# Kernel optimization log

Hardware: AMD Instinct MI355X
Metric: run time of the kernel (lower is better)

Reference implementation:

```python
import jax, jax.numpy as jnp
import numpy as np

N = 100000   # nodes
E = 1600000  # edges
G = 512      # graphs
H = 128      # hidden = dim_features
T = 10       # dim_target
L = 4        # no_layers (first_h + 3 GINConvs)
BN_EPS = 1e-5


def setup_inputs() -> dict:
    key = jax.random.key(0)
    ks = jax.random.split(key, 12)
    s = 1.0 / np.sqrt(H)
    inp = {
        "x": jax.random.normal(ks[0], (N, H), jnp.float32),
        "edge_index": jax.random.randint(ks[1], (2, E), 0, N, jnp.int64),
        "batch": jnp.sort(jax.random.randint(ks[2], (N,), 0, G, jnp.int64)),
        "Wa": jax.random.normal(ks[3], (L, H, H), jnp.float32) * s,
        "ba": jax.random.normal(ks[4], (L, H), jnp.float32) * s,
        "ga": jnp.ones((L, H), jnp.float32),
        "bea": jnp.zeros((L, H), jnp.float32),
        "Wb": jax.random.normal(ks[5], (L, H, H), jnp.float32) * s,
        "bb": jax.random.normal(ks[6], (L, H), jnp.float32) * s,
        "gb": jnp.ones((L, H), jnp.float32),
        "beb": jnp.zeros((L, H), jnp.float32),
        "Wl": jax.random.normal(ks[7], (L, H, T), jnp.float32) * s,
        "bl": jax.random.normal(ks[8], (L, T), jnp.float32) * s,
        "eps": jnp.zeros((3,), jnp.float32),
    }
    return inp


def _bn(h, g, b):
    # BatchNorm1d in training mode: batch stats over node dim, biased var
    mu = jnp.mean(h, axis=0)
    var = jnp.mean(jnp.square(h - mu), axis=0)
    return g * (h - mu) * jax.lax.rsqrt(var + BN_EPS) + b


def _mlp(h, l, Wa, ba, ga, bea, Wb, bb, gb, beb):
    # Linear -> BN -> ReLU -> Linear -> BN -> ReLU
    h = jax.nn.relu(_bn(h @ Wa[l] + ba[l], ga[l], bea[l]))
    h = jax.nn.relu(_bn(h @ Wb[l] + bb[l], gb[l], beb[l]))
    return h


def _mean_pool(v, batch):
    sums = jax.ops.segment_sum(v, batch, num_segments=G)
    cnt = jax.ops.segment_sum(jnp.ones((v.shape[0], 1), v.dtype), batch, num_segments=G)
    return sums / jnp.maximum(cnt, 1.0)


def reference(x, edge_index, batch, Wa, ba, ga, bea, Wb, bb, gb, beb, Wl, bl, eps):
    src, dst = edge_index[0], edge_index[1]
    # layer 0: first_h MLP, then linear -> pool
    h = _mlp(x, 0, Wa, ba, ga, bea, Wb, bb, gb, beb)
    out = _mean_pool(h @ Wl[0] + bl[0], batch)
    # layers 1..3: GINConv = MLP((1+eps)*x + sum_{j->i} x_j), then pool -> linear
    for l in range(1, L):
        agg = jax.ops.segment_sum(h[src], dst, num_segments=N)  # scatter-add over edges
        h = _mlp((1.0 + eps[l - 1]) * h + agg, l, Wa, ba, ga, bea, Wb, bb, gb, beb)
        out = out + _mean_pool(h, batch) @ Wl[l] + bl[l]
    return jax.nn.sigmoid(out.reshape(-1))  # [G*T]
```

## Files before the change

### kernel.cpp

```cpp
#include <hip/hip_runtime.h>
#include <hip/hip_bf16.h>

#define N_      100000
#define E_      1600000
#define G_      512
#define H_      128
#define T_      10
#define BN_EPS  1e-5f
#define SP_     16

#define NB_     782
#define NBLK_   256
#define ECHUNK_ 6250
#define SCANN_  (NB_ * NBLK_)
#define SCANB_  ((SCANN_ + 1023) / 1024)

typedef __attribute__((ext_vector_type(8))) short short8;
typedef __attribute__((ext_vector_type(4))) float floatx4;

__device__ __forceinline__ float bf2f(short s) {
    return __uint_as_float(((unsigned int)(unsigned short)s) << 16);
}
__device__ __forceinline__ short f2bf(float f) {
    unsigned int u = __float_as_uint(f);
    u += 0x7fffu + ((u >> 16) & 1u);
    return (short)(u >> 16);
}

__global__ __launch_bounds__(256) void prep(
    const float* __restrict__ Wa, const float* __restrict__ Wb,
    short* __restrict__ Wt, const int* __restrict__ edst,
    int* __restrict__ BH)
{
    __shared__ int hist[NB_];
    const int t = threadIdx.x, blk = blockIdx.x;
    for (int i = t; i < NB_; i += 256) hist[i] = 0;
    __syncthreads();

    for (int i = blk * 256 + t; i < 8 * 16384; i += NBLK_ * 256) {
        int mat = i >> 14;
        int rem = i & 16383;
        int n = rem >> 7;
        int k = rem & 127;
        const float* W = (mat < 4) ? (Wa + (size_t)mat * 16384)
                                   : (Wb + (size_t)(mat - 4) * 16384);
        Wt[(size_t)mat * 16384 + n * 128 + k] = f2bf(W[k * 128 + n]);
    }
    const int base = blk * ECHUNK_;
    for (int i = base + t; i < base + ECHUNK_; i += 256)
        atomicAdd(&hist[edst[i] >> 7], 1);
    __syncthreads();
    for (int b = t; b < NB_; b += 256)
        BH[b * NBLK_ + blk] = hist[b];
}

__global__ __launch_bounds__(256) void scan1(const int* __restrict__ X,
                                             int* __restrict__ Y,
                                             int* __restrict__ bsum, int n)
{
    __shared__ int sd[256];
    int t = threadIdx.x;
    int base = blockIdx.x * 1024 + t * 4;
    int c0 = (base + 0 < n) ? X[base + 0] : 0;
    int c1 = (base + 1 < n) ? X[base + 1] : 0;
    int c2 = (base + 2 < n) ? X[base + 2] : 0;
    int c3 = (base + 3 < n) ? X[base + 3] : 0;
    int s = c0 + c1 + c2 + c3;
    sd[t] = s;
    __syncthreads();
    for (int d = 1; d < 256; d <<= 1) {
        int v = (t >= d) ? sd[t - d] : 0;
        __syncthreads();
        sd[t] += v;
        __syncthreads();
    }
    int p = sd[t] - s;
    if (base + 0 < n) Y[base + 0] = p;
    if (base + 1 < n) Y[base + 1] = p + c0;
    if (base + 2 < n) Y[base + 2] = p + c0 + c1;
    if (base + 3 < n) Y[base + 3] = p + c0 + c1 + c2;
    if (t == 255) bsum[blockIdx.x] = sd[255];
}

__device__ __forceinline__ void scan_bsum(const int* __restrict__ bsum,
                                          int* bexcl)
{
    int t = threadIdx.x;
    int v = (t < SCANB_) ? bsum[t] : 0;
    bexcl[t] = v;
    __syncthreads();
    for (int d = 1; d < 256; d <<= 1) {
        int u = (t >= d) ? bexcl[t - d] : 0;
        __syncthreads();
        bexcl[t] += u;
        __syncthreads();
    }
    int inc = bexcl[t];
    __syncthreads();
    bexcl[t] = inc - v;
    __syncthreads();
}

__global__ __launch_bounds__(256) void scatter_ebuf(
    const int* __restrict__ esrc, const int* __restrict__ edst,
    const int* __restrict__ BHs, const int* __restrict__ bsum,
    int* __restrict__ ebuf)
{
    __shared__ int sbuf[NB_];
    __shared__ int bexcl[256];
    const int t = threadIdx.x, blk = blockIdx.x;
    scan_bsum(bsum, bexcl);
    for (int b = t; b < NB_; b += 256)
        sbuf[b] = BHs[b * NBLK_ + blk] + bexcl[b >> 2];
    __syncthreads();
    const int base = blk * ECHUNK_;
    for (int i = base + t; i < base + ECHUNK_; i += 256) {
        int s = esrc[i], d = edst[i];
        int pos = atomicAdd(&sbuf[d >> 7], 1);
        ebuf[pos] = s | ((d & 127) << 17);
    }
}

__global__ __launch_bounds__(256) void fill_buckets(
    const int* __restrict__ ebuf, const int* __restrict__ BHs,
    const int* __restrict__ bsum, int* __restrict__ eidx,
    int* __restrict__ off)
{
    __shared__ int cnt[128];
    __shared__ int sc[256];
    __shared__ int bexcl[256];
    const int b = blockIdx.x, t = threadIdx.x;
    scan_bsum(bsum, bexcl);
    const int bstart = BHs[b * NBLK_] + bexcl[b >> 2];
    int bend = E_;
    if (b != NB_ - 1)
        bend = BHs[(b + 1) * NBLK_] + bexcl[(b + 1) >> 2];

    if (t < 128) cnt[t] = 0;
    __syncthreads();
    for (int i = bstart + t; i < bend; i += 256)
        atomicAdd(&cnt[(ebuf[i] >> 17) & 127], 1);
    __syncthreads();
    int v = (t < 128) ? cnt[t] : 0;
    sc[t] = v;
    __syncthreads();
    for (int d = 1; d < 128; d <<= 1) {
        int u = (t >= d) ? sc[t - d] : 0;
        __syncthreads();
        sc[t] += u;
        __syncthreads();
    }
    if (t < 128) {
        int node = (b << 7) + t;
        int pfx = sc[t] - v;
        if (node <= N_) off[node] = bstart + pfx;
        cnt[t] = bstart + pfx;
    }
    __syncthreads();
    for (int i = bstart + t; i < bend; i += 256) {
        int e = ebuf[i];
        int pos = atomicAdd(&cnt[(e >> 17) & 127], 1);
        eidx[pos] = e & 0x1FFFF;
    }
}

__global__ __launch_bounds__(512, 6) void gemm_mfma(
    const void* __restrict__ Ain, const short* __restrict__ Wt,
    const float* __restrict__ bias, short* __restrict__ Cout,
    float* __restrict__ statsOut,
    const float* __restrict__ statsIn, const float* __restrict__ gamma,
    const float* __restrict__ beta, int mode, int nrows)
{
    __shared__ __align__(16) short Bs[128][136];
    __shared__ float scale_s[128];
    __shared__ float shift_s[128];

    const int tid = threadIdx.x;

    {
        int r = tid >> 2;
        int part = (tid & 3) << 5;
        const short* g = Wt + r * 128 + part;
        short* d = &Bs[r][part];
#pragma unroll
        for (int i = 0; i < 4; ++i)
            *(short8*)(d + i * 8) = *(const short8*)(g + i * 8);
    }
    if (mode == 1 && tid < 128) {
        float s1 = 0.f, s2 = 0.f;
#pragma unroll
        for (int p = 0; p < SP_; ++p) {
            s1 += statsIn[p * 256 + tid];
            s2 += statsIn[p * 256 + 128 + tid];
        }
        const float nInv = 1.0f / (float)N_;
        float mu = s1 * nInv;
        float var = s2 * nInv - mu * mu;
        float sc = gamma[tid] * rsqrtf(var + BN_EPS);
        scale_s[tid] = sc;
        shift_s[tid] = beta[tid] - mu * sc;
    }
    __syncthreads();

    const int wave = tid >> 6;
    const int lane = tid & 63;
    const int m = lane & 15;
    const int quad = lane >> 4;
    const int rowBase = blockIdx.x * 128;
    const int row = rowBase + wave * 16 + m;
    const int arow = row < nrows ? row : nrows - 1;

    floatx4 acc[8];
#pragma unroll
    for (int i = 0; i < 8; ++i) acc[i] = (floatx4)0.f;

#pragma unroll
    for (int k0 = 0; k0 < 128; k0 += 32) {
        const int kb = k0 + quad * 8;
        short8 af;
        if (mode == 2) {
            const float* Af = (const float*)Ain + (size_t)arow * 128 + kb;
            float4 x0 = *(const float4*)(Af);
            float4 x1 = *(const float4*)(Af + 4);
            af[0] = f2bf(x0.x); af[1] = f2bf(x0.y);
            af[2] = f2bf(x0.z); af[3] = f2bf(x0.w);
            af[4] = f2bf(x1.x); af[5] = f2bf(x1.y);
            af[6] = f2bf(x1.z); af[7] = f2bf(x1.w);
        } else {
            af = *(const short8*)((const short*)Ain + (size_t)arow * 128 + kb);
            if (mode == 1) {
                float4 sc0 = *(const float4*)&scale_s[kb];
                float4 sc1 = *(const float4*)&scale_s[kb + 4];
                float4 sh0 = *(const float4*)&shift_s[kb];
                float4 sh1 = *(const float4*)&shift_s[kb + 4];
                af[0] = f2bf(fmaxf(fmaf(bf2f(af[0]), sc0.x, sh0.x), 0.f));
                af[1] = f2bf(fmaxf(fmaf(bf2f(af[1]), sc0.y, sh0.y), 0.f));
                af[2] = f2bf(fmaxf(fmaf(bf2f(af[2]), sc0.z, sh0.z), 0.f));
                af[3] = f2bf(fmaxf(fmaf(bf2f(af[3]), sc0.w, sh0.w), 0.f));
                af[4] = f2bf(fmaxf(fmaf(bf2f(af[4]), sc1.x, sh1.x), 0.f));
                af[5] = f2bf(fmaxf(fmaf(bf2f(af[5]), sc1.y, sh1.y), 0.f));
                af[6] = f2bf(fmaxf(fmaf(bf2f(af[6]), sc1.z, sh1.z), 0.f));
                af[7] = f2bf(fmaxf(fmaf(bf2f(af[7]), sc1.w, sh1.w), 0.f));
            }
        }
#pragma unroll
        for (int nt = 0; nt < 8; ++nt) {
            short8 bf = *(const short8*)&Bs[nt * 16 + m][kb];
            acc[nt] = __builtin_amdgcn_mfma_f32_16x16x32_bf16(af, bf, acc[nt], 0, 0, 0);
        }
    }

    float bv[8];
#pragma unroll
    for (int nt = 0; nt < 8; ++nt) bv[nt] = bias[nt * 16 + m];

    float (*Cs)[132] = (float(*)[132])&Bs[0][0];
    float S1 = 0.f, S2 = 0.f;
#pragma unroll
    for (int half = 0; half < 2; ++half) {
        __syncthreads();
        if ((wave >> 2) == half) {
            int wl = wave & 3;
#pragma unroll
            for (int nt = 0; nt < 8; ++nt)
#pragma unroll
                for (int r = 0; r < 4; ++r)
                    Cs[wl * 16 + quad * 4 + r][nt * 16 + m] = acc[nt][r] + bv[nt];
        }
        __syncthreads();
        {
            int trow = tid >> 3;
            int tcg = (tid & 7) << 4;
            int grow = rowBase + half * 64 + trow;
            if (grow < nrows) {
                short* dst = Cout + (size_t)grow * 128 + tcg;
                short8 o0, o1;
#pragma unroll
                for (int j = 0; j < 8; ++j) {
                    o0[j] = f2bf(Cs[trow][tcg + j]);
                    o1[j] = f2bf(Cs[trow][tcg + 8 + j]);
                }
                *(short8*)dst = o0;
                *(short8*)(dst + 8) = o1;
            }
        }
        if (tid < 128) {
            int nvalid = nrows - rowBase - half * 64;
            if (nvalid > 64) nvalid = 64;
            for (int r = 0; r < nvalid; ++r) {
                float v = Cs[r][tid];
                S1 += v; S2 += v * v;
            }
        }
    }
    if (tid < 128) {
        float* part = statsOut + ((blockIdx.x & (SP_ - 1)) << 8);
        atomicAdd(&part[tid], S1);
        atomicAdd(&part[128 + tid], S2);
    }
}

__global__ __launch_bounds__(128) void bn_relu_pool(
    const short* __restrict__ Cin, short* __restrict__ hout,
    const float* __restrict__ stats, const float* __restrict__ gamma,
    const float* __restrict__ beta, const int* __restrict__ batch,
    float* __restrict__ pooled, int n)
{
    int c = threadIdx.x;
    float s1 = 0.f, s2 = 0.f;
#pragma unroll
    for (int p = 0; p < SP_; ++p) {
        s1 += stats[p * 256 + c];
        s2 += stats[p * 256 + 128 + c];
    }
    const float nInv = 1.0f / (float)N_;
    float mu = s1 * nInv;
    float var = s2 * nInv - mu * mu;
    float sc = gamma[c] * rsqrtf(var + BN_EPS);
    float sh = beta[c] - mu * sc;

    int per = (n + gridDim.x - 1) / gridDim.x;
    int r0 = blockIdx.x * per;
    int r1 = min(n, r0 + per);
    if (r0 >= r1) return;
    int curg = batch[r0];
    float s = 0.f;
    if (hout) {
        for (int r = r0; r < r1; ++r) {
            int g = batch[r];
            if (g != curg) {
                atomicAdd(&pooled[(size_t)curg * 128 + c], s);
                s = 0.f;
                curg = g;
            }
            float v = fmaxf(fmaf(bf2f(Cin[(size_t)r * 128 + c]), sc, sh), 0.f);
            hout[(size_t)r * 128 + c] = f2bf(v);
            s += v;
        }
    } else {
        for (int r = r0; r < r1; ++r) {
            int g = batch[r];
            if (g != curg) {
                atomicAdd(&pooled[(size_t)curg * 128 + c], s);
                s = 0.f;
                curg = g;
            }
            s += fmaxf(fmaf(bf2f(Cin[(size_t)r * 128 + c]), sc, sh), 0.f);
        }
    }
    atomicAdd(&pooled[(size_t)curg * 128 + c], s);
}

__global__ __launch_bounds__(256) void aggregate(
    const short* __restrict__ h, short* __restrict__ u,
    const int* __restrict__ off, const int* __restrict__ eidx,
    const float* __restrict__ eps, int li)
{
    int node = blockIdx.x * 4 + (threadIdx.x >> 6);
    if (node >= N_) return;
    int lane = threadIdx.x & 63;
    int col = lane * 2;

    int s0 = off[node];
    int s1 = off[node + 1];
    float se = 1.0f + eps[li];

    ushort2 a = *(const ushort2*)(h + (size_t)node * 128 + col);
    float ax = bf2f((short)a.x) * se;
    float ay = bf2f((short)a.y) * se;

    int j = s0;
    for (; j + 3 < s1; j += 4) {
        int n0 = eidx[j], n1 = eidx[j + 1], n2 = eidx[j + 2], n3 = eidx[j + 3];
        ushort2 v0 = *(const ushort2*)(h + (size_t)n0 * 128 + col);
        ushort2 v1 = *(const ushort2*)(h + (size_t)n1 * 128 + col);
        ushort2 v2 = *(const ushort2*)(h + (size_t)n2 * 128 + col);
        ushort2 v3 = *(const ushort2*)(h + (size_t)n3 * 128 + col);
        ax += (bf2f((short)v0.x) + bf2f((short)v1.x))
            + (bf2f((short)v2.x) + bf2f((short)v3.x));
        ay += (bf2f((short)v0.y) + bf2f((short)v1.y))
            + (bf2f((short)v2.y) + bf2f((short)v3.y));
    }
    for (; j < s1; ++j) {
        int n0 = eidx[j];
        ushort2 v0 = *(const ushort2*)(h + (size_t)n0 * 128 + col);
        ax += bf2f((short)v0.x);
        ay += bf2f((short)v0.y);
    }
    unsigned int o = (unsigned int)(unsigned short)f2bf(ax)
                   | ((unsigned int)(unsigned short)f2bf(ay) << 16);
    __builtin_nontemporal_store(o, (unsigned int*)(u + (size_t)node * 128 + col));
}

__global__ void out_final(const float* __restrict__ pooled,
                          const int* __restrict__ batch,
                          const float* __restrict__ Wl,
                          const float* __restrict__ bl, float* __restrict__ out)
{
    int g = blockIdx.x;
    int t = threadIdx.x;
    if (t >= T_) return;
    int lo = 0, hi = N_;
    while (lo < hi) { int mid = (lo + hi) >> 1; if (batch[mid] < g) lo = mid + 1; else hi = mid; }
    int b0 = lo;
    lo = 0; hi = N_;
    while (lo < hi) { int mid = (lo + hi) >> 1; if (batch[mid] < g + 1) lo = mid + 1; else hi = mid; }
    float inv = 1.0f / fmaxf((float)(lo - b0), 1.0f);
    float acc = 0.f;
#pragma unroll
    for (int l = 0; l < 4; ++l) {
        float s = 0.f;
        for (int c = 0; c < 128; ++c)
            s = fmaf(pooled[(size_t)l * (G_ * H_) + g * 128 + c],
                     Wl[(size_t)l * (H_ * T_) + c * T_ + t], s);
        acc += s * inv + bl[l * T_ + t];
    }
    out[g * T_ + t] = 1.0f / (1.0f + expf(-acc));
}

extern "C" void kernel_launch(void* const* d_in, const int* in_sizes, int n_in,
                              void* d_out, int out_size, void* d_ws, size_t ws_size,
                              hipStream_t stream)
{
    const float* x    = (const float*)d_in[0];
    const int*   ei   = (const int*)d_in[1];
    const int*   batch= (const int*)d_in[2];
    const float* Wa   = (const float*)d_in[3];
    const float* ba   = (const float*)d_in[4];
    const float* ga   = (const float*)d_in[5];
    const float* bea  = (const float*)d_in[6];
    const float* Wb   = (const float*)d_in[7];
    const float* bb   = (const float*)d_in[8];
    const float* gb   = (const float*)d_in[9];
    const float* beb  = (const float*)d_in[10];
    const float* Wl   = (const float*)d_in[11];
    const float* bl   = (const float*)d_in[12];
    const float* eps  = (const float*)d_in[13];
    float* out = (float*)d_out;

    const size_t NH = (size_t)N_ * H_;
    const int statStride = SP_ * 256;
    short* A   = (short*)d_ws;
    short* B   = A + NH;
    short* C   = B + NH;
    short* Wt  = C + NH;
    float* stats  = (float*)(Wt + 8 * 16384);
    float* pooled = stats + 8 * statStride;
    int*   BH     = (int*)(pooled + 4 * (size_t)G_ * H_);
    int*   BHs    = BH + SCANN_;
    int*   bsum   = BHs + SCANN_;
    int*   off    = bsum + 256;
    int*   ebuf   = off + 100352;
    int*   eidx   = ebuf + E_;

    const size_t zbytes = (size_t)(8 * statStride + 4 * G_ * H_) * 4;
    (void)hipMemsetAsync(stats, 0, zbytes, stream);

    const int* esrc = ei;
    const int* edst = ei + E_;

    prep<<<NBLK_, 256, 0, stream>>>(Wa, Wb, Wt, edst, BH);
    scan1<<<SCANB_, 256, 0, stream>>>(BH, BHs, bsum, SCANN_);
    scatter_ebuf<<<NBLK_, 256, 0, stream>>>(esrc, edst, BHs, bsum, ebuf);
    fill_buckets<<<NB_, 256, 0, stream>>>(ebuf, BHs, bsum, eidx, off);

    const int gemmGrid = (N_ + 127) / 128;
    const int aggGrid  = (N_ + 3) / 4;

    gemm_mfma<<<gemmGrid, 512, 0, stream>>>(x, Wt, ba, A, stats,
                                            nullptr, nullptr, nullptr, 2, N_);
    gemm_mfma<<<gemmGrid, 512, 0, stream>>>(A, Wt + 4 * 16384, bb, B,
                                            stats + statStride,
                                            stats, ga, bea, 1, N_);
    bn_relu_pool<<<1024, 128, 0, stream>>>(B, C, stats + statStride, gb, beb,
                                           batch, pooled, N_);

    for (int l = 1; l < 4; ++l) {
        float* stA = stats + (size_t)(2 * l) * statStride;
        float* stB = stats + (size_t)(2 * l + 1) * statStride;
        aggregate<<<aggGrid, 256, 0, stream>>>(C, A, off, eidx, eps, l - 1);
        gemm_mfma<<<gemmGrid, 512, 0, stream>>>(A, Wt + (size_t)l * 16384,
                                                ba + l * H_, B, stA,
                                                nullptr, nullptr, nullptr, 0, N_);
        gemm_mfma<<<gemmGrid, 512, 0, stream>>>(B, Wt + (size_t)(4 + l) * 16384,
                                                bb + l * H_, A, stB,
                                                stA, ga + l * H_, bea + l * H_, 1, N_);
        bn_relu_pool<<<1024, 128, 0, stream>>>(A, (l < 3) ? C : nullptr, stB,
                                               gb + l * H_, beb + l * H_,
                                               batch, pooled + (size_t)l * G_ * H_, N_);
    }

    out_final<<<G_, 64, 0, stream>>>(pooled, batch, Wl, bl, out);
}
```

Baseline: 678.6 us.

## Piggyback edge bucketing stages onto layer-0 GEMM and pool launches

Runs the edge-destination histogram, prefix scan and edge scatter as extra side blocks appended to the first two GEMM launches and the first BN/ReLU/pool launch. Only weight conversion stays a separate small kernel. The aim is to overlap the graph CSR construction with independent dense work and cut launch count and serialization. The pool kernel is widened to 256 threads with two virtual row ranges per block to match the scatter's block shape. The side blocks compete for CUs and LDS with the GEMM and can lengthen its tail.

```diff
diff --git a/kernel.cpp b/kernel.cpp
--- a/kernel.cpp
+++ b/kernel.cpp
@@ -14,6 +14,7 @@
 #define ECHUNK_ 6250
 #define SCANN_  (NB_ * NBLK_)
 #define SCANB_  ((SCANN_ + 1023) / 1024)
+#define POOLB_  512
 
 typedef __attribute__((ext_vector_type(8))) short short8;
 typedef __attribute__((ext_vector_type(4))) float floatx4;
@@ -27,59 +28,55 @@
     return (short)(u >> 16);
 }
 
-__global__ __launch_bounds__(256) void prep(
+__global__ __launch_bounds__(256) void convert_W(
     const float* __restrict__ Wa, const float* __restrict__ Wb,
-    short* __restrict__ Wt, const int* __restrict__ edst,
-    int* __restrict__ BH)
-{
-    __shared__ int hist[NB_];
-    const int t = threadIdx.x, blk = blockIdx.x;
-    for (int i = t; i < NB_; i += 256) hist[i] = 0;
-    __syncthreads();
-
-    for (int i = blk * 256 + t; i < 8 * 16384; i += NBLK_ * 256) {
-        int mat = i >> 14;
-        int rem = i & 16383;
-        int n = rem >> 7;
-        int k = rem & 127;
-        const float* W = (mat < 4) ? (Wa + (size_t)mat * 16384)
-                                   : (Wb + (size_t)(mat - 4) * 16384);
-        Wt[(size_t)mat * 16384 + n * 128 + k] = f2bf(W[k * 128 + n]);
-    }
+    short* __restrict__ Wt)
+{
+    int i = blockIdx.x * 256 + threadIdx.x;
+    if (i >= 8 * 16384) return;
+    int mat = i >> 14;
+    int rem = i & 16383;
+    int n = rem >> 7;
+    int k = rem & 127;
+    const float* W = (mat < 4) ? (Wa + (size_t)mat * 16384)
+                               : (Wb + (size_t)(mat - 4) * 16384);
+    Wt[(size_t)mat * 16384 + n * 128 + k] = f2bf(W[k * 128 + n]);
+}
+
+__device__ void side_hist(int* hist, const int* __restrict__ edst,
+                          int* __restrict__ BH, int blk)
+{
+    const int t = threadIdx.x;
+    for (int i = t; i < NB_; i += 512) hist[i] = 0;
+    __syncthreads();
     const int base = blk * ECHUNK_;
-    for (int i = base + t; i < base + ECHUNK_; i += 256)
+    for (int i = base + t; i < base + ECHUNK_; i += 512)
         atomicAdd(&hist[edst[i] >> 7], 1);
     __syncthreads();
-    for (int b = t; b < NB_; b += 256)
+    for (int b = t; b < NB_; b += 512)
         BH[b * NBLK_ + blk] = hist[b];
 }
 
-__global__ __launch_bounds__(256) void scan1(const int* __restrict__ X,
-                                             int* __restrict__ Y,
-                                             int* __restrict__ bsum, int n)
-{
-    __shared__ int sd[256];
-    int t = threadIdx.x;
-    int base = blockIdx.x * 1024 + t * 4;
-    int c0 = (base + 0 < n) ? X[base + 0] : 0;
-    int c1 = (base + 1 < n) ? X[base + 1] : 0;
-    int c2 = (base + 2 < n) ? X[base + 2] : 0;
-    int c3 = (base + 3 < n) ? X[base + 3] : 0;
-    int s = c0 + c1 + c2 + c3;
+__device__ void side_scan(int* sd, const int* __restrict__ X,
+                          int* __restrict__ Y, int* __restrict__ bsum, int blk)
+{
+    const int t = threadIdx.x;
+    const int base = blk * 1024 + t * 2;
+    int c0 = (base + 0 < SCANN_) ? X[base + 0] : 0;
+    int c1 = (base + 1 < SCANN_) ? X[base + 1] : 0;
+    int s = c0 + c1;
     sd[t] = s;
     __syncthreads();
-    for (int d = 1; d < 256; d <<= 1) {
+    for (int d = 1; d < 512; d <<= 1) {
         int v = (t >= d) ? sd[t - d] : 0;
         __syncthreads();
         sd[t] += v;
         __syncthreads();
     }
     int p = sd[t] - s;
-    if (base + 0 < n) Y[base + 0] = p;
-    if (base + 1 < n) Y[base + 1] = p + c0;
-    if (base + 2 < n) Y[base + 2] = p + c0 + c1;
-    if (base + 3 < n) Y[base + 3] = p + c0 + c1 + c2;
-    if (t == 255) bsum[blockIdx.x] = sd[255];
+    if (base + 0 < SCANN_) Y[base + 0] = p;
+    if (base + 1 < SCANN_) Y[base + 1] = p + c0;
+    if (t == 511) bsum[blk] = sd[511];
 }
 
 __device__ __forceinline__ void scan_bsum(const int* __restrict__ bsum,
@@ -99,26 +96,6 @@
     __syncthreads();
     bexcl[t] = inc - v;
     __syncthreads();
-}
-
-__global__ __launch_bounds__(256) void scatter_ebuf(
-    const int* __restrict__ esrc, const int* __restrict__ edst,
-    const int* __restrict__ BHs, const int* __restrict__ bsum,
-    int* __restrict__ ebuf)
-{
-    __shared__ int sbuf[NB_];
-    __shared__ int bexcl[256];
-    const int t = threadIdx.x, blk = blockIdx.x;
-    scan_bsum(bsum, bexcl);
-    for (int b = t; b < NB_; b += 256)
-        sbuf[b] = BHs[b * NBLK_ + blk] + bexcl[b >> 2];
-    __syncthreads();
-    const int base = blk * ECHUNK_;
-    for (int i = base + t; i < base + ECHUNK_; i += 256) {
-        int s = esrc[i], d = edst[i];
-        int pos = atomicAdd(&sbuf[d >> 7], 1);
-        ebuf[pos] = s | ((d & 127) << 17);
-    }
 }
 
 __global__ __launch_bounds__(256) void fill_buckets(
@@ -169,13 +146,22 @@
     const float* __restrict__ bias, short* __restrict__ Cout,
     float* __restrict__ statsOut,
     const float* __restrict__ statsIn, const float* __restrict__ gamma,
-    const float* __restrict__ beta, int mode, int nrows)
+    const float* __restrict__ beta, int mode, int nrows,
+    const int* __restrict__ sideIn, int* __restrict__ sideOut,
+    int* __restrict__ sideOut2, int sideMode, int gemmBlocks)
 {
     __shared__ __align__(16) short Bs[128][136];
     __shared__ float scale_s[128];
     __shared__ float shift_s[128];
 
     const int tid = threadIdx.x;
+
+    if ((int)blockIdx.x >= gemmBlocks) {
+        int sb = blockIdx.x - gemmBlocks;
+        if (sideMode == 1)      side_hist((int*)&Bs[0][0], sideIn, sideOut, sb);
+        else if (sideMode == 2) side_scan((int*)&Bs[0][0], sideIn, sideOut, sideOut2, sb);
+        return;
+    }
 
     {
         int r = tid >> 2;
@@ -300,13 +286,35 @@
     }
 }
 
-__global__ __launch_bounds__(128) void bn_relu_pool(
+__global__ __launch_bounds__(256) void bn_relu_pool(
     const short* __restrict__ Cin, short* __restrict__ hout,
     const float* __restrict__ stats, const float* __restrict__ gamma,
     const float* __restrict__ beta, const int* __restrict__ batch,
-    float* __restrict__ pooled, int n)
-{
-    int c = threadIdx.x;
+    float* __restrict__ pooled, int n,
+    const int* __restrict__ esrc, const int* __restrict__ edst,
+    const int* __restrict__ BHs, const int* __restrict__ bsum,
+    int* __restrict__ ebuf, int poolBlocks)
+{
+    __shared__ int sbuf[NB_];
+    __shared__ int bexcl[256];
+    const int tid = threadIdx.x;
+
+    if ((int)blockIdx.x >= poolBlocks) {
+        int blk = blockIdx.x - poolBlocks;
+        scan_bsum(bsum, bexcl);
+        for (int b = tid; b < NB_; b += 256)
+            sbuf[b] = BHs[b * NBLK_ + blk] + bexcl[b >> 2];
+        __syncthreads();
+        const int base = blk * ECHUNK_;
+        for (int i = base + tid; i < base + ECHUNK_; i += 256) {
+            int s = esrc[i], d = edst[i];
+            int pos = atomicAdd(&sbuf[d >> 7], 1);
+            ebuf[pos] = s | ((d & 127) << 17);
+        }
+        return;
+    }
+
+    const int c = tid & 127;
     float s1 = 0.f, s2 = 0.f;
 #pragma unroll
     for (int p = 0; p < SP_; ++p) {
@@ -319,8 +327,10 @@
     float sc = gamma[c] * rsqrtf(var + BN_EPS);
     float sh = beta[c] - mu * sc;
 
-    int per = (n + gridDim.x - 1) / gridDim.x;
-    int r0 = blockIdx.x * per;
+    const int nv = poolBlocks * 2;
+    const int vblk = blockIdx.x * 2 + (tid >> 7);
+    int per = (n + nv - 1) / nv;
+    int r0 = vblk * per;
     int r1 = min(n, r0 + per);
     if (r0 >= r1) return;
     int curg = batch[r0];
@@ -459,35 +469,39 @@
     const int* esrc = ei;
     const int* edst = ei + E_;
 
-    prep<<<NBLK_, 256, 0, stream>>>(Wa, Wb, Wt, edst, BH);
-    scan1<<<SCANB_, 256, 0, stream>>>(BH, BHs, bsum, SCANN_);
-    scatter_ebuf<<<NBLK_, 256, 0, stream>>>(esrc, edst, BHs, bsum, ebuf);
-    fill_buckets<<<NB_, 256, 0, stream>>>(ebuf, BHs, bsum, eidx, off);
-
     const int gemmGrid = (N_ + 127) / 128;
     const int aggGrid  = (N_ + 3) / 4;
 
-    gemm_mfma<<<gemmGrid, 512, 0, stream>>>(x, Wt, ba, A, stats,
-                                            nullptr, nullptr, nullptr, 2, N_);
-    gemm_mfma<<<gemmGrid, 512, 0, stream>>>(A, Wt + 4 * 16384, bb, B,
-                                            stats + statStride,
-                                            stats, ga, bea, 1, N_);
-    bn_relu_pool<<<1024, 128, 0, stream>>>(B, C, stats + statStride, gb, beb,
-                                           batch, pooled, N_);
+    convert_W<<<512, 256, 0, stream>>>(Wa, Wb, Wt);
+
+    gemm_mfma<<<gemmGrid + NBLK_, 512, 0, stream>>>(
+        x, Wt, ba, A, stats, nullptr, nullptr, nullptr, 2, N_,
+        edst, BH, nullptr, 1, gemmGrid);
+    gemm_mfma<<<gemmGrid + SCANB_, 512, 0, stream>>>(
+        A, Wt + 4 * 16384, bb, B, stats + statStride,
+        stats, ga, bea, 1, N_,
+        BH, BHs, bsum, 2, gemmGrid);
+    bn_relu_pool<<<POOLB_ + NBLK_, 256, 0, stream>>>(
+        B, C, stats + statStride, gb, beb, batch, pooled, N_,
+        esrc, edst, BHs, bsum, ebuf, POOLB_);
+    fill_buckets<<<NB_, 256, 0, stream>>>(ebuf, BHs, bsum, eidx, off);
 
     for (int l = 1; l < 4; ++l) {
         float* stA = stats + (size_t)(2 * l) * statStride;
         float* stB = stats + (size_t)(2 * l + 1) * statStride;
         aggregate<<<aggGrid, 256, 0, stream>>>(C, A, off, eidx, eps, l - 1);
-        gemm_mfma<<<gemmGrid, 512, 0, stream>>>(A, Wt + (size_t)l * 16384,
-                                                ba + l * H_, B, stA,
-                                                nullptr, nullptr, nullptr, 0, N_);
-        gemm_mfma<<<gemmGrid, 512, 0, stream>>>(B, Wt + (size_t)(4 + l) * 16384,
-                                                bb + l * H_, A, stB,
-                                                stA, ga + l * H_, bea + l * H_, 1, N_);
-        bn_relu_pool<<<1024, 128, 0, stream>>>(A, (l < 3) ? C : nullptr, stB,
-                                               gb + l * H_, beb + l * H_,
-                                               batch, pooled + (size_t)l * G_ * H_, N_);
+        gemm_mfma<<<gemmGrid, 512, 0, stream>>>(
+            A, Wt + (size_t)l * 16384, ba + l * H_, B, stA,
+            nullptr, nullptr, nullptr, 0, N_,
+            nullptr, nullptr, nullptr, 0, gemmGrid);
+        gemm_mfma<<<gemmGrid, 512, 0, stream>>>(
+            B, Wt + (size_t)(4 + l) * 16384, bb + l * H_, A, stB,
+            stA, ga + l * H_, bea + l * H_, 1, N_,
+            nullptr, nullptr, nullptr, 0, gemmGrid);
+        bn_relu_pool<<<POOLB_, 256, 0, stream>>>(
+            A, (l < 3) ? C : nullptr, stB, gb + l * H_, beb + l * H_,
+            batch, pooled + (size_t)l * G_ * H_, N_,
+            nullptr, nullptr, nullptr, nullptr, nullptr, POOLB_);
     }
 
     out_final<<<G_, 64, 0, stream>>>(pooled, batch, Wl, bl, out);
```

After: 742.2 us. 9.4% more time.
